# Optimization experiments

Measured on AMD Instinct MI355X. Metric: run time of the kernel, lower is better.

## Reference

```python
import jax, jax.numpy as jnp
import numpy as np

N_NODES = 50000
N_EDGES = 800000
HIDDEN = 128
HEADS = 8
HEAD_DIM = HIDDEN // HEADS


def setup_inputs() -> dict:
    key = jax.random.key(0)
    ks = jax.random.split(key, 9)
    h = jax.random.normal(ks[0], (N_NODES, HIDDEN), dtype=jnp.float32)
    src = jax.random.randint(ks[1], (N_EDGES,), 0, N_NODES, dtype=jnp.int64)
    dst = jax.random.randint(ks[2], (N_EDGES,), 0, N_NODES, dtype=jnp.int64)
    s = 1.0 / np.sqrt(HIDDEN)
    WQ_w = jax.random.normal(ks[3], (HIDDEN, HIDDEN), dtype=jnp.float32) * s
    WQ_b = jax.random.normal(ks[4], (HIDDEN,), dtype=jnp.float32) * 0.01
    WK_w = jax.random.normal(ks[5], (HIDDEN, HIDDEN), dtype=jnp.float32) * s
    WK_b = jax.random.normal(ks[6], (HIDDEN,), dtype=jnp.float32) * 0.01
    WV_w = jax.random.normal(ks[7], (HIDDEN, HIDDEN), dtype=jnp.float32) * s
    WV_b = jax.random.normal(ks[8], (HIDDEN,), dtype=jnp.float32) * 0.01
    return {"h": h, "src": src, "dst": dst,
            "WQ_w": WQ_w, "WQ_b": WQ_b,
            "WK_w": WK_w, "WK_b": WK_b,
            "WV_w": WV_w, "WV_b": WV_b}


def reference(h, src, dst, WQ_w, WQ_b, WK_w, WK_b, WV_w, WV_b):
    n = h.shape[0]
    scale = jnp.sqrt(jnp.asarray(HEAD_DIM, dtype=h.dtype))
    # QKV projections (torch Linear: x @ W.T + b), reshape to [N, H, D]
    Q = (h @ WQ_w.T + WQ_b).reshape(n, HEADS, HEAD_DIM)
    K = (h @ WK_w.T + WK_b).reshape(n, HEADS, HEAD_DIM)
    V = (h @ WV_w.T + WV_b).reshape(n, HEADS, HEAD_DIM)
    # per-edge scores: (Q[dst] * K[src]).sum(-1) / scale  -> [E, H]
    scores = jnp.einsum("ehd,ehd->eh", Q[dst], K[src]) / scale
    # segment softmax over incoming edges of each dst node
    m = jax.ops.segment_max(scores, dst, num_segments=n)          # [N, H]
    e = jnp.exp(scores - m[dst])                                   # [E, H]
    denom = jax.ops.segment_sum(e, dst, num_segments=n)           # [N, H]
    attn = e / denom[dst]                                          # [E, H]
    # weighted V aggregation: [E,H,1]*[E,H,D] scattered to dst -> [N,H,D]
    out = jax.ops.segment_sum(attn[:, :, None] * V[src], dst, num_segments=n)
    return out  # [N, HEADS, HEAD_DIM]
```

## Files before the change

### kernel.cpp

```cpp
#include <hip/hip_runtime.h>
#include <hip/hip_bf16.h>
#include <cstdint>

#define HID 128
#define NH 8
#define HD 16

typedef __attribute__((ext_vector_type(8))) short bf16x8;
typedef __attribute__((ext_vector_type(4))) float f32x4;

#if __has_builtin(__builtin_amdgcn_exp2f)
#define EXP2(x) __builtin_amdgcn_exp2f(x)
#else
#define EXP2(x) exp2f(x)
#endif

__device__ __forceinline__ short bfr(float x) {
  return (short)__bfloat16_as_ushort(__float2bfloat16(x));
}

__device__ __forceinline__ void up2(uint32_t w, float& lo, float& hi) {
  lo = __uint_as_float(w << 16);
  hi = __uint_as_float(w & 0xffff0000u);
}

__global__ __launch_bounds__(256) void fill_conv_kernel(
    const int* __restrict__ src, const int* __restrict__ dst,
    int* __restrict__ cursors, int* __restrict__ buckets, int E, int C,
    const float* __restrict__ W0, const float* __restrict__ W1,
    const float* __restrict__ W2, short* __restrict__ Wb) {
  int e = blockIdx.x * 256 + threadIdx.x;
  if (e < E) {
    int d = dst[e];
    int pos = atomicAdd(&cursors[d], 1);
    if (pos < C) buckets[(size_t)d * C + pos] = src[e];
  }
  if (e < 3 * HID * HID) {
    int mat = e >> 14;
    int j = e & 16383;
    const float* W = (mat == 0) ? W0 : (mat == 1) ? W1 : W2;
    Wb[e] = bfr(W[j]);
  }
}

__global__ __launch_bounds__(256) void qkv_mfma(
    const float* __restrict__ h, const short* __restrict__ Wb,
    const float* __restrict__ b0, const float* __restrict__ b1,
    const float* __restrict__ b2,
    ushort* __restrict__ Q, ushort* __restrict__ K, ushort* __restrict__ V,
    int n) {
  __shared__ short As[16 * 64 * 8];
  const int tid = threadIdx.x;
  const int m0 = blockIdx.x * 64;

  {
    const int row = tid >> 2, q = tid & 3;
    const int gm = m0 + row;
    const bool ok = gm < n;
    const float4* hp = (const float4*)(h + (size_t)gm * HID + q * 32);
#pragma unroll
    for (int j2 = 0; j2 < 4; ++j2) {
      float4 a = ok ? hp[2 * j2] : make_float4(0.f, 0.f, 0.f, 0.f);
      float4 b = ok ? hp[2 * j2 + 1] : make_float4(0.f, 0.f, 0.f, 0.f);
      bf16x8 c;
      c[0] = bfr(a.x); c[1] = bfr(a.y); c[2] = bfr(a.z); c[3] = bfr(a.w);
      c[4] = bfr(b.x); c[5] = bfr(b.y); c[6] = bfr(b.z); c[7] = bfr(b.w);
      int ch = q * 4 + j2;
      *(bf16x8*)&As[(ch * 64 + row) * 8] = c;
    }
  }
  __syncthreads();

  const int lane = tid & 63;
  const int w = tid >> 6;
  const int r16 = lane & 15;
  const int kg = lane >> 4;

  const float* bms[3] = {b0, b1, b2};
  ushort* Oms[3] = {Q, K, V};

#pragma unroll
  for (int mat = 0; mat < 3; ++mat) {
    f32x4 acc[2][4] = {};
#pragma unroll
    for (int ks = 0; ks < 4; ++ks) {
      bf16x8 wfrag[2];
#pragma unroll
      for (int ct = 0; ct < 2; ++ct) {
        int gc = mat * HID + w * 32 + ct * 16 + r16;
        wfrag[ct] = *(const bf16x8*)(Wb + (size_t)gc * HID + ks * 32 + kg * 8);
      }
#pragma unroll
      for (int rt = 0; rt < 4; ++rt) {
        bf16x8 hfrag = *(const bf16x8*)&As[((ks * 4 + kg) * 64 + rt * 16 + r16) * 8];
#pragma unroll
        for (int ct = 0; ct < 2; ++ct)
          acc[ct][rt] = __builtin_amdgcn_mfma_f32_16x16x32_bf16(wfrag[ct], hfrag, acc[ct][rt], 0, 0, 0);
      }
    }
    const float* bm = bms[mat];
    ushort* Om = Oms[mat];
#pragma unroll
    for (int ct = 0; ct < 2; ++ct) {
      const int col0 = w * 32 + ct * 16 + kg * 4;
      const float4 bias = *(const float4*)(bm + col0);
#pragma unroll
      for (int rt = 0; rt < 4; ++rt) {
        int gm = m0 + rt * 16 + r16;
        if (gm < n) {
          float c0 = acc[ct][rt][0] + bias.x;
          float c1 = acc[ct][rt][1] + bias.y;
          float c2 = acc[ct][rt][2] + bias.z;
          float c3 = acc[ct][rt][3] + bias.w;
          uint2 u;
          u.x = (uint32_t)__bfloat16_as_ushort(__float2bfloat16(c0)) |
                ((uint32_t)__bfloat16_as_ushort(__float2bfloat16(c1)) << 16);
          u.y = (uint32_t)__bfloat16_as_ushort(__float2bfloat16(c2)) |
                ((uint32_t)__bfloat16_as_ushort(__float2bfloat16(c3)) << 16);
          *(uint2*)(Om + (size_t)gm * HID + col0) = u;
        }
      }
    }
  }
}

__global__ __launch_bounds__(256) void agg_kernel(
    const char* __restrict__ Qb, const char* __restrict__ Kb,
    const char* __restrict__ Vb,
    const int* __restrict__ cursors, const int* __restrict__ buckets, int C,
    float* __restrict__ out, int n) {
  const int tid = threadIdx.x;
  const int lane = tid & 63;
  const int node = blockIdx.x * 4 + (tid >> 6);
  if (node >= n) return;

  const int q = lane >> 4;
  const int sub = lane & 15;
  const int so = sub << 4;

  const float S = 0.25f * 1.44269504f;
  uint4 qw = *(const uint4*)(Qb + (((size_t)node) << 8) + so);
  float qf0, qf1, qf2, qf3, qf4, qf5, qf6, qf7;
  up2(qw.x, qf0, qf1); up2(qw.y, qf2, qf3);
  up2(qw.z, qf4, qf5); up2(qw.w, qf6, qf7);
  qf0 *= S; qf1 *= S; qf2 *= S; qf3 *= S;
  qf4 *= S; qf5 *= S; qf6 *= S; qf7 *= S;

  const int deg = min(cursors[node], C);
  const int* bk = buckets + (size_t)node * C;
  int2 myidx = *(const int2*)(bk + ((sub & 7) << 3) + (q << 1));

  float m_r = -1e30f, sum_r = 0.f;
  float a0 = 0.f, a1 = 0.f, a2 = 0.f, a3 = 0.f;
  float a4 = 0.f, a5 = 0.f, a6 = 0.f, a7 = 0.f;

  const int nit = (deg + 7) >> 3;
  for (int it = 0; it < nit; ++it) {
    const int srcl = (lane & 48) | it;
    const int i0 = __shfl(myidx.x, srcl);
    const int i1 = __shfl(myidx.y, srcl);
    const int e0 = it * 8 + 2 * q, e1 = e0 + 1;
    const uint32_t s0 = min((uint32_t)i0, (uint32_t)(n - 1));
    const uint32_t s1 = min((uint32_t)i1, (uint32_t)(n - 1));
    const uint4 k0 = *(const uint4*)(Kb + (((size_t)s0) << 8) + so);
    const uint4 k1 = *(const uint4*)(Kb + (((size_t)s1) << 8) + so);
    const uint4 v0w = *(const uint4*)(Vb + (((size_t)s0) << 8) + so);
    const uint4 v1w = *(const uint4*)(Vb + (((size_t)s1) << 8) + so);

    float x0, x1;
    up2(k0.x, x0, x1); float p0 = qf0 * x0 + qf1 * x1;
    up2(k0.y, x0, x1); p0 += qf2 * x0 + qf3 * x1;
    up2(k0.z, x0, x1); p0 += qf4 * x0 + qf5 * x1;
    up2(k0.w, x0, x1); p0 += qf6 * x0 + qf7 * x1;
    up2(k1.x, x0, x1); float p1 = qf0 * x0 + qf1 * x1;
    up2(k1.y, x0, x1); p1 += qf2 * x0 + qf3 * x1;
    up2(k1.z, x0, x1); p1 += qf4 * x0 + qf5 * x1;
    up2(k1.w, x0, x1); p1 += qf6 * x0 + qf7 * x1;
    p0 += __shfl_xor(p0, 1);
    p1 += __shfl_xor(p1, 1);
    p0 = (e0 < deg) ? p0 : -INFINITY;
    p1 = (e1 < deg) ? p1 : -INFINITY;

    const float mn = fmaxf(m_r, fmaxf(p0, p1));
    const float scale = EXP2(m_r - mn);
    const float w0 = EXP2(p0 - mn);
    const float w1 = EXP2(p1 - mn);
    m_r = mn;
    sum_r = sum_r * scale + w0 + w1;
    float y0, y1, z0, z1;
    up2(v0w.x, y0, y1); up2(v1w.x, z0, z1);
    a0 = a0 * scale + w0 * y0 + w1 * z0; a1 = a1 * scale + w0 * y1 + w1 * z1;
    up2(v0w.y, y0, y1); up2(v1w.y, z0, z1);
    a2 = a2 * scale + w0 * y0 + w1 * z0; a3 = a3 * scale + w0 * y1 + w1 * z1;
    up2(v0w.z, y0, y1); up2(v1w.z, z0, z1);
    a4 = a4 * scale + w0 * y0 + w1 * z0; a5 = a5 * scale + w0 * y1 + w1 * z1;
    up2(v0w.w, y0, y1); up2(v1w.w, z0, z1);
    a6 = a6 * scale + w0 * y0 + w1 * z0; a7 = a7 * scale + w0 * y1 + w1 * z1;
  }

  float mo = fmaxf(m_r, __shfl_xor(m_r, 16));
  mo = fmaxf(mo, __shfl_xor(mo, 32));
  const float sc = EXP2(m_r - mo);
  float s_all = sum_r * sc;
  s_all += __shfl_xor(s_all, 16);
  s_all += __shfl_xor(s_all, 32);
  a0 *= sc; a1 *= sc; a2 *= sc; a3 *= sc;
  a4 *= sc; a5 *= sc; a6 *= sc; a7 *= sc;
  a0 += __shfl_xor(a0, 16); a1 += __shfl_xor(a1, 16);
  a2 += __shfl_xor(a2, 16); a3 += __shfl_xor(a3, 16);
  a4 += __shfl_xor(a4, 16); a5 += __shfl_xor(a5, 16);
  a6 += __shfl_xor(a6, 16); a7 += __shfl_xor(a7, 16);
  a0 += __shfl_xor(a0, 32); a1 += __shfl_xor(a1, 32);
  a2 += __shfl_xor(a2, 32); a3 += __shfl_xor(a3, 32);
  a4 += __shfl_xor(a4, 32); a5 += __shfl_xor(a5, 32);
  a6 += __shfl_xor(a6, 32); a7 += __shfl_xor(a7, 32);

  if (q == 0) {
    const float inv = (s_all > 0.f) ? 1.f / s_all : 0.f;
    float* orow = out + (((size_t)node) << 7) + (sub << 3);
    *(float4*)orow = make_float4(a0 * inv, a1 * inv, a2 * inv, a3 * inv);
    *(float4*)(orow + 4) = make_float4(a4 * inv, a5 * inv, a6 * inv, a7 * inv);
  }
}


extern "C" void kernel_launch(void* const* d_in, const int* in_sizes, int n_in,
                              void* d_out, int out_size, void* d_ws, size_t ws_size,
                              hipStream_t stream) {
  const float* h  = (const float*)d_in[0];
  const int* src  = (const int*)d_in[1];
  const int* dst  = (const int*)d_in[2];
  const float* WQ = (const float*)d_in[3];
  const float* bQ = (const float*)d_in[4];
  const float* WK = (const float*)d_in[5];
  const float* bK = (const float*)d_in[6];
  const float* WV = (const float*)d_in[7];
  const float* bV = (const float*)d_in[8];
  float* out = (float*)d_out;

  const int n = in_sizes[0] / HID;
  const int E = in_sizes[1];

  ushort* Q = (ushort*)d_ws;
  ushort* K = Q + (size_t)n * HID;
  ushort* V = K + (size_t)n * HID;
  short* Wb = (short*)(V + (size_t)n * HID);
  int* cursors = (int*)(Wb + 384 * HID);
  int* buckets = cursors + n;

  const size_t fixed = ((size_t)3 * n * HID + 384 * HID) * 2 + (size_t)n * 4;
  int C = 64;
  if (fixed + ((size_t)n * 64 + 64) * 4 > ws_size) C = 48;
  if (fixed + ((size_t)n * 48 + 64) * 4 > ws_size) C = 40;

  hipMemsetAsync(cursors, 0, (size_t)n * sizeof(int), stream);
  fill_conv_kernel<<<(E + 255) / 256, 256, 0, stream>>>(src, dst, cursors, buckets,
                                                        E, C, WQ, WK, WV, Wb);
  qkv_mfma<<<(n + 63) / 64, 256, 0, stream>>>(h, Wb, bQ, bK, bV, Q, K, V, n);
  agg_kernel<<<(n + 3) / 4, 256, 0, stream>>>((const char*)Q, (const char*)K,
                                              (const char*)V, cursors, buckets, C, out, n);
}
```

Measured before the change: 150.0 us.

## Merge bucket fill and QKV projection into one launch, interleave K and V rows

Measured after the change: 169.8 us. 13.2% more time.

```diff
diff --git a/kernel.cpp b/kernel.cpp
--- a/kernel.cpp
+++ b/kernel.cpp
@@ -24,34 +24,28 @@
   hi = __uint_as_float(w & 0xffff0000u);
 }
 
-__global__ __launch_bounds__(256) void fill_conv_kernel(
+__global__ __launch_bounds__(256) void prep_kernel(
     const int* __restrict__ src, const int* __restrict__ dst,
-    int* __restrict__ cursors, int* __restrict__ buckets, int E, int C,
-    const float* __restrict__ W0, const float* __restrict__ W1,
-    const float* __restrict__ W2, short* __restrict__ Wb) {
-  int e = blockIdx.x * 256 + threadIdx.x;
-  if (e < E) {
-    int d = dst[e];
-    int pos = atomicAdd(&cursors[d], 1);
-    if (pos < C) buckets[(size_t)d * C + pos] = src[e];
-  }
-  if (e < 3 * HID * HID) {
-    int mat = e >> 14;
-    int j = e & 16383;
-    const float* W = (mat == 0) ? W0 : (mat == 1) ? W1 : W2;
-    Wb[e] = bfr(W[j]);
-  }
-}
-
-__global__ __launch_bounds__(256) void qkv_mfma(
-    const float* __restrict__ h, const short* __restrict__ Wb,
-    const float* __restrict__ b0, const float* __restrict__ b1,
-    const float* __restrict__ b2,
-    ushort* __restrict__ Q, ushort* __restrict__ K, ushort* __restrict__ V,
-    int n) {
+    int* __restrict__ cursors, int* __restrict__ buckets, int E, int C, int FB,
+    const float* __restrict__ h,
+    const float* __restrict__ W0, const float* __restrict__ b0,
+    const float* __restrict__ W1, const float* __restrict__ b1,
+    const float* __restrict__ W2, const float* __restrict__ b2,
+    ushort* __restrict__ Q, ushort* __restrict__ KV, int n) {
+  const int tid = threadIdx.x;
+
+  if (blockIdx.x < (unsigned)FB) {
+    int e = blockIdx.x * 256 + tid;
+    if (e < E) {
+      int d = dst[e];
+      int pos = atomicAdd(&cursors[d], 1);
+      if (pos < C) buckets[(size_t)d * C + pos] = src[e];
+    }
+    return;
+  }
+
   __shared__ short As[16 * 64 * 8];
-  const int tid = threadIdx.x;
-  const int m0 = blockIdx.x * 64;
+  const int m0 = (blockIdx.x - FB) * 64;
 
   {
     const int row = tid >> 2, q = tid & 3;
@@ -76,19 +70,26 @@
   const int r16 = lane & 15;
   const int kg = lane >> 4;
 
+  const float* Wms[3] = {W0, W1, W2};
   const float* bms[3] = {b0, b1, b2};
-  ushort* Oms[3] = {Q, K, V};
 
 #pragma unroll
   for (int mat = 0; mat < 3; ++mat) {
+    const float* Wm = Wms[mat];
     f32x4 acc[2][4] = {};
 #pragma unroll
     for (int ks = 0; ks < 4; ++ks) {
       bf16x8 wfrag[2];
 #pragma unroll
       for (int ct = 0; ct < 2; ++ct) {
-        int gc = mat * HID + w * 32 + ct * 16 + r16;
-        wfrag[ct] = *(const bf16x8*)(Wb + (size_t)gc * HID + ks * 32 + kg * 8);
+        const int gr = w * 32 + ct * 16 + r16;
+        const float* wrow = Wm + (size_t)gr * HID + ks * 32 + kg * 8;
+        float4 wa = *(const float4*)wrow;
+        float4 wb = *(const float4*)(wrow + 4);
+        bf16x8 wf;
+        wf[0] = bfr(wa.x); wf[1] = bfr(wa.y); wf[2] = bfr(wa.z); wf[3] = bfr(wa.w);
+        wf[4] = bfr(wb.x); wf[5] = bfr(wb.y); wf[6] = bfr(wb.z); wf[7] = bfr(wb.w);
+        wfrag[ct] = wf;
       }
 #pragma unroll
       for (int rt = 0; rt < 4; ++rt) {
@@ -99,7 +100,8 @@
       }
     }
     const float* bm = bms[mat];
-    ushort* Om = Oms[mat];
+    ushort* base = (mat == 0) ? Q : (mat == 1) ? KV : (KV + HID);
+    const int rs = (mat == 0) ? HID : 2 * HID;
 #pragma unroll
     for (int ct = 0; ct < 2; ++ct) {
       const int col0 = w * 32 + ct * 16 + kg * 4;
@@ -117,7 +119,7 @@
                 ((uint32_t)__bfloat16_as_ushort(__float2bfloat16(c1)) << 16);
           u.y = (uint32_t)__bfloat16_as_ushort(__float2bfloat16(c2)) |
                 ((uint32_t)__bfloat16_as_ushort(__float2bfloat16(c3)) << 16);
-          *(uint2*)(Om + (size_t)gm * HID + col0) = u;
+          *(uint2*)(base + (size_t)gm * rs + col0) = u;
         }
       }
     }
@@ -125,8 +127,7 @@
 }
 
 __global__ __launch_bounds__(256) void agg_kernel(
-    const char* __restrict__ Qb, const char* __restrict__ Kb,
-    const char* __restrict__ Vb,
+    const char* __restrict__ Qb, const char* __restrict__ KVb,
     const int* __restrict__ cursors, const int* __restrict__ buckets, int C,
     float* __restrict__ out, int n) {
   const int tid = threadIdx.x;
@@ -162,10 +163,12 @@
     const int e0 = it * 8 + 2 * q, e1 = e0 + 1;
     const uint32_t s0 = min((uint32_t)i0, (uint32_t)(n - 1));
     const uint32_t s1 = min((uint32_t)i1, (uint32_t)(n - 1));
-    const uint4 k0 = *(const uint4*)(Kb + (((size_t)s0) << 8) + so);
-    const uint4 k1 = *(const uint4*)(Kb + (((size_t)s1) << 8) + so);
-    const uint4 v0w = *(const uint4*)(Vb + (((size_t)s0) << 8) + so);
-    const uint4 v1w = *(const uint4*)(Vb + (((size_t)s1) << 8) + so);
+    const size_t rb0 = ((size_t)s0) << 9;
+    const size_t rb1 = ((size_t)s1) << 9;
+    const uint4 k0 = *(const uint4*)(KVb + rb0 + so);
+    const uint4 k1 = *(const uint4*)(KVb + rb1 + so);
+    const uint4 v0w = *(const uint4*)(KVb + rb0 + 256 + so);
+    const uint4 v1w = *(const uint4*)(KVb + rb1 + 256 + so);
 
     float x0, x1;
     up2(k0.x, x0, x1); float p0 = qf0 * x0 + qf1 * x1;
@@ -240,23 +243,22 @@
 
   const int n = in_sizes[0] / HID;
   const int E = in_sizes[1];
-
-  ushort* Q = (ushort*)d_ws;
-  ushort* K = Q + (size_t)n * HID;
-  ushort* V = K + (size_t)n * HID;
-  short* Wb = (short*)(V + (size_t)n * HID);
-  int* cursors = (int*)(Wb + 384 * HID);
+  const int FB = (E + 255) / 256;
+  const int QB = (n + 63) / 64;
+
+  ushort* Q  = (ushort*)d_ws;
+  ushort* KV = Q + (size_t)n * HID;
+  int* cursors = (int*)(KV + (size_t)n * 2 * HID);
   int* buckets = cursors + n;
 
-  const size_t fixed = ((size_t)3 * n * HID + 384 * HID) * 2 + (size_t)n * 4;
+  const size_t fixed = (size_t)n * (HID + 2 * HID) * 2 + (size_t)n * 4;
   int C = 64;
   if (fixed + ((size_t)n * 64 + 64) * 4 > ws_size) C = 48;
   if (fixed + ((size_t)n * 48 + 64) * 4 > ws_size) C = 40;
 
   hipMemsetAsync(cursors, 0, (size_t)n * sizeof(int), stream);
-  fill_conv_kernel<<<(E + 255) / 256, 256, 0, stream>>>(src, dst, cursors, buckets,
-                                                        E, C, WQ, WK, WV, Wb);
-  qkv_mfma<<<(n + 63) / 64, 256, 0, stream>>>(h, Wb, bQ, bK, bV, Q, K, V, n);
-  agg_kernel<<<(n + 3) / 4, 256, 0, stream>>>((const char*)Q, (const char*)K,
-                                              (const char*)V, cursors, buckets, C, out, n);
-}
+  prep_kernel<<<FB + QB, 256, 0, stream>>>(src, dst, cursors, buckets, E, C, FB,
+                                           h, WQ, bQ, WK, bK, WV, bV, Q, KV, n);
+  agg_kernel<<<(n + 3) / 4, 256, 0, stream>>>((const char*)Q, (const char*)KV,
+                                              cursors, buckets, C, out, n);
+}
```

## Interleave K and V rows and vectorize edge bucketing by four

Applied to the files above, without the earlier changes.

Result: faster. 144.1 us (-4.0%).

```diff
diff --git a/kernel.cpp b/kernel.cpp
--- a/kernel.cpp
+++ b/kernel.cpp
@@ -29,17 +29,37 @@
     int* __restrict__ cursors, int* __restrict__ buckets, int E, int C,
     const float* __restrict__ W0, const float* __restrict__ W1,
     const float* __restrict__ W2, short* __restrict__ Wb) {
-  int e = blockIdx.x * 256 + threadIdx.x;
-  if (e < E) {
-    int d = dst[e];
-    int pos = atomicAdd(&cursors[d], 1);
-    if (pos < C) buckets[(size_t)d * C + pos] = src[e];
-  }
-  if (e < 3 * HID * HID) {
-    int mat = e >> 14;
-    int j = e & 16383;
+  const int t = blockIdx.x * 256 + threadIdx.x;
+  const int e0 = t * 4;
+  if (e0 + 3 < E) {
+    const int4 d4 = *(const int4*)(dst + e0);
+    const int4 s4 = *(const int4*)(src + e0);
+    int p0 = atomicAdd(&cursors[d4.x], 1);
+    int p1 = atomicAdd(&cursors[d4.y], 1);
+    int p2 = atomicAdd(&cursors[d4.z], 1);
+    int p3 = atomicAdd(&cursors[d4.w], 1);
+    if (p0 < C) buckets[(size_t)d4.x * C + p0] = s4.x;
+    if (p1 < C) buckets[(size_t)d4.y * C + p1] = s4.y;
+    if (p2 < C) buckets[(size_t)d4.z * C + p2] = s4.z;
+    if (p3 < C) buckets[(size_t)d4.w * C + p3] = s4.w;
+  } else {
+    for (int e = e0; e < E; ++e) {
+      int d = dst[e];
+      int pos = atomicAdd(&cursors[d], 1);
+      if (pos < C) buckets[(size_t)d * C + pos] = src[e];
+    }
+  }
+  if (t < 3 * HID * HID / 8) {
+    const int base = t * 8;
+    const int mat = base >> 14;
+    const int j = base & 16383;
     const float* W = (mat == 0) ? W0 : (mat == 1) ? W1 : W2;
-    Wb[e] = bfr(W[j]);
+    float4 a = *(const float4*)(W + j);
+    float4 b = *(const float4*)(W + j + 4);
+    bf16x8 c;
+    c[0] = bfr(a.x); c[1] = bfr(a.y); c[2] = bfr(a.z); c[3] = bfr(a.w);
+    c[4] = bfr(b.x); c[5] = bfr(b.y); c[6] = bfr(b.z); c[7] = bfr(b.w);
+    *(bf16x8*)(Wb + base) = c;
   }
 }
 
@@ -47,8 +67,7 @@
     const float* __restrict__ h, const short* __restrict__ Wb,
     const float* __restrict__ b0, const float* __restrict__ b1,
     const float* __restrict__ b2,
-    ushort* __restrict__ Q, ushort* __restrict__ K, ushort* __restrict__ V,
-    int n) {
+    ushort* __restrict__ Q, ushort* __restrict__ KV, int n) {
   __shared__ short As[16 * 64 * 8];
   const int tid = threadIdx.x;
   const int m0 = blockIdx.x * 64;
@@ -77,7 +96,6 @@
   const int kg = lane >> 4;
 
   const float* bms[3] = {b0, b1, b2};
-  ushort* Oms[3] = {Q, K, V};
 
 #pragma unroll
   for (int mat = 0; mat < 3; ++mat) {
@@ -99,7 +117,8 @@
       }
     }
     const float* bm = bms[mat];
-    ushort* Om = Oms[mat];
+    ushort* base = (mat == 0) ? Q : (mat == 1) ? KV : (KV + HID);
+    const int rs = (mat == 0) ? HID : 2 * HID;
 #pragma unroll
     for (int ct = 0; ct < 2; ++ct) {
       const int col0 = w * 32 + ct * 16 + kg * 4;
@@ -117,7 +136,7 @@
                 ((uint32_t)__bfloat16_as_ushort(__float2bfloat16(c1)) << 16);
           u.y = (uint32_t)__bfloat16_as_ushort(__float2bfloat16(c2)) |
                 ((uint32_t)__bfloat16_as_ushort(__float2bfloat16(c3)) << 16);
-          *(uint2*)(Om + (size_t)gm * HID + col0) = u;
+          *(uint2*)(base + (size_t)gm * rs + col0) = u;
         }
       }
     }
@@ -125,8 +144,7 @@
 }
 
 __global__ __launch_bounds__(256) void agg_kernel(
-    const char* __restrict__ Qb, const char* __restrict__ Kb,
-    const char* __restrict__ Vb,
+    const char* __restrict__ Qb, const char* __restrict__ KVb,
     const int* __restrict__ cursors, const int* __restrict__ buckets, int C,
     float* __restrict__ out, int n) {
   const int tid = threadIdx.x;
@@ -162,10 +180,12 @@
     const int e0 = it * 8 + 2 * q, e1 = e0 + 1;
     const uint32_t s0 = min((uint32_t)i0, (uint32_t)(n - 1));
     const uint32_t s1 = min((uint32_t)i1, (uint32_t)(n - 1));
-    const uint4 k0 = *(const uint4*)(Kb + (((size_t)s0) << 8) + so);
-    const uint4 k1 = *(const uint4*)(Kb + (((size_t)s1) << 8) + so);
-    const uint4 v0w = *(const uint4*)(Vb + (((size_t)s0) << 8) + so);
-    const uint4 v1w = *(const uint4*)(Vb + (((size_t)s1) << 8) + so);
+    const size_t rb0 = ((size_t)s0) << 9;
+    const size_t rb1 = ((size_t)s1) << 9;
+    const uint4 k0 = *(const uint4*)(KVb + rb0 + so);
+    const uint4 k1 = *(const uint4*)(KVb + rb1 + so);
+    const uint4 v0w = *(const uint4*)(KVb + rb0 + 256 + so);
+    const uint4 v1w = *(const uint4*)(KVb + rb1 + 256 + so);
 
     float x0, x1;
     up2(k0.x, x0, x1); float p0 = qf0 * x0 + qf1 * x1;
@@ -241,22 +261,22 @@
   const int n = in_sizes[0] / HID;
   const int E = in_sizes[1];
 
-  ushort* Q = (ushort*)d_ws;
-  ushort* K = Q + (size_t)n * HID;
-  ushort* V = K + (size_t)n * HID;
-  short* Wb = (short*)(V + (size_t)n * HID);
+  ushort* Q  = (ushort*)d_ws;
+  ushort* KV = Q + (size_t)n * HID;
+  short* Wb = (short*)(KV + (size_t)n * 2 * HID);
   int* cursors = (int*)(Wb + 384 * HID);
   int* buckets = cursors + n;
 
-  const size_t fixed = ((size_t)3 * n * HID + 384 * HID) * 2 + (size_t)n * 4;
+  const size_t fixed = (size_t)n * 384 * 2 + 384 * HID * 2 + (size_t)n * 4;
   int C = 64;
   if (fixed + ((size_t)n * 64 + 64) * 4 > ws_size) C = 48;
   if (fixed + ((size_t)n * 48 + 64) * 4 > ws_size) C = 40;
 
+  const int nt4 = (E + 3) / 4;
   hipMemsetAsync(cursors, 0, (size_t)n * sizeof(int), stream);
-  fill_conv_kernel<<<(E + 255) / 256, 256, 0, stream>>>(src, dst, cursors, buckets,
-                                                        E, C, WQ, WK, WV, Wb);
-  qkv_mfma<<<(n + 63) / 64, 256, 0, stream>>>(h, Wb, bQ, bK, bV, Q, K, V, n);
-  agg_kernel<<<(n + 3) / 4, 256, 0, stream>>>((const char*)Q, (const char*)K,
-                                              (const char*)V, cursors, buckets, C, out, n);
-}
+  fill_conv_kernel<<<(nt4 + 255) / 256, 256, 0, stream>>>(src, dst, cursors, buckets,
+                                                          E, C, WQ, WK, WV, Wb);
+  qkv_mfma<<<(n + 63) / 64, 256, 0, stream>>>(h, Wb, bQ, bK, bV, Q, KV, n);
+  agg_kernel<<<(n + 3) / 4, 256, 0, stream>>>((const char*)Q, (const char*)KV,
+                                              cursors, buckets, C, out, n);
+}
```
